# Performance work log

Measured on AMD Instinct MI355X. Metric: run time of the kernel, lower is better.

The kernel has to match this reference:

```python
import jax, jax.numpy as jnp
import numpy as np

B, S, H, F, E, K, R = 1, 1024, 1024, 4096, 8, 2, 16
SCALING = 2.0  # lora_alpha / lora_r = 32 / 16


def setup_inputs() -> dict:
    key = jax.random.key(0)
    ks = jax.random.split(key, 14)
    rnd = lambda i, shape, scale=0.02: (jax.random.normal(ks[i], shape, jnp.float32) * scale)
    return {
        "hidden_states": rnd(0, (B, S, H), 1.0),
        "noise": rnd(1, (B * S, E), 1.0),          # stands in for torch.randn_like(logits)
        "w_route": rnd(2, (H, E)),                   # gate.topkroute_linear.weight^T
        "w_noise": rnd(3, (H, E)),                   # gate.noise_linear.weight^T
        "w_gate": rnd(4, (H, F)),                    # shared mlp gate_proj
        "w_up": rnd(5, (H, F)),                      # shared mlp up_proj
        "w_down": rnd(6, (F, H)),                    # shared mlp down_proj
        "a_gate": rnd(7, (E, H, R)),                 # per-expert LoRA A/B on gate_proj
        "b_gate": rnd(8, (E, R, F)),
        "a_up": rnd(9, (E, H, R)),
        "b_up": rnd(10, (E, R, F)),
        "a_down": rnd(11, (E, F, R)),
        "b_down": rnd(12, (E, R, H)),
    }


def reference(hidden_states, noise, w_route, w_noise, w_gate, w_up, w_down,
              a_gate, b_gate, a_up, b_up, a_down, b_down):
    Bx, Sx, Hx = hidden_states.shape
    x = hidden_states.reshape(-1, Hx)                       # [T, H]
    T = x.shape[0]

    # NoisyTopkRouter
    logits = x @ w_route                                     # [T, E]
    noise_logits = x @ w_noise
    router_logits = logits + noise * jax.nn.softplus(noise_logits)

    # softmax in fp32, top-k, renormalize
    probs = jax.nn.softmax(router_logits.astype(jnp.float32), axis=-1)
    rw, sel = jax.lax.top_k(probs, K)                        # [T, K]
    rw = rw / rw.sum(axis=-1, keepdims=True)
    rw = rw.astype(x.dtype)

    # dense per-(token, expert) combine weights (equiv. to the gather/index_add loop)
    wdense = jnp.zeros((T, E), x.dtype).at[jnp.arange(T)[:, None], sel].add(rw)  # [T, E]

    # LoRA experts (Mixtral MLP shared `mlp` + per-expert low-rank adapters), vectorized over E
    gate = jnp.einsum('th,hf->tf', x, w_gate)[None] + SCALING * jnp.einsum('th,ehr,erf->etf', x, a_gate, b_gate)  # [E,T,F]
    up = jnp.einsum('th,hf->tf', x, w_up)[None] + SCALING * jnp.einsum('th,ehr,erf->etf', x, a_up, b_up)          # [E,T,F]
    act = jax.nn.silu(gate) * up                                                                                   # [E,T,F]
    down = jnp.einsum('etf,fh->eth', act, w_down) + SCALING * jnp.einsum('etf,efr,erh->eth', act, a_down, b_down)  # [E,T,H]

    out = jnp.einsum('te,eth->th', wdense, down)             # scatter-add combine
    return out.reshape(Bx, Sx, Hx), router_logits
```

## Files before the change

### kernel.cpp

```cpp
#include <hip/hip_runtime.h>
#include <hip/hip_bf16.h>

typedef __hip_bfloat16 bf16;
typedef __attribute__((ext_vector_type(4))) float f32x4;
typedef __attribute__((ext_vector_type(8))) __bf16 bf16x8;

#define T_TOK 1024
#define HDIM 1024
#define FDIM 4096
#define NEXP 8
#define RLORA 16
#define LSCALE 2.0f
#define N1 8448
#define N2 1152
#define SPLITK2 4
#define ACT_NCHUNK 8

__device__ inline float b2f(bf16 v) { return __bfloat162float(v); }
__device__ inline bf16 f2b(float v) { return __float2bfloat16(v); }
__device__ inline ushort f2u(float v) { return __builtin_bit_cast(ushort, __float2bfloat16(v)); }
__device__ inline float u2f(ushort v) { return __bfloat162float(__builtin_bit_cast(bf16, v)); }
__device__ inline float lo2f(unsigned w) { return __builtin_bit_cast(float, w << 16); }
__device__ inline float hi2f(unsigned w) { return __builtin_bit_cast(float, w & 0xffff0000u); }

typedef const __attribute__((address_space(1))) unsigned int* gptr_t;
typedef __attribute__((address_space(3))) unsigned int* lptr_t;
__device__ __forceinline__ void glds16(const void* g, void* l) {
    __builtin_amdgcn_global_load_lds((gptr_t)g, (lptr_t)l, 16, 0, 0);
}

__global__ __launch_bounds__(256) void router_kernel(
    const float* __restrict__ x, const float* __restrict__ noise,
    const float* __restrict__ w_route, const float* __restrict__ w_noise,
    float* __restrict__ rl_out, int* __restrict__ SEL, float* __restrict__ WTS,
    int* __restrict__ CNT, int* __restrict__ LIST)
{
    const int t = blockIdx.x, tid = threadIdx.x;
    const float* xr = x + t * HDIM;
    float acc[16];
#pragma unroll
    for (int j = 0; j < 16; j++) acc[j] = 0.f;
    for (int h = tid; h < HDIM; h += 256) {
        float xv = xr[h];
        const float* wr = w_route + h * NEXP;
        const float* wn = w_noise + h * NEXP;
#pragma unroll
        for (int j = 0; j < 8; j++) acc[j] += xv * wr[j];
#pragma unroll
        for (int j = 0; j < 8; j++) acc[8 + j] += xv * wn[j];
    }
#pragma unroll
    for (int j = 0; j < 16; j++) {
        for (int off = 32; off > 0; off >>= 1) acc[j] += __shfl_down(acc[j], off, 64);
    }
    __shared__ float red[4][16];
    const int wave = tid >> 6, lane = tid & 63;
    if (lane == 0) {
#pragma unroll
        for (int j = 0; j < 16; j++) red[wave][j] = acc[j];
    }
    __syncthreads();
    if (tid == 0) {
        float rl[8];
#pragma unroll
        for (int j = 0; j < 8; j++) {
            float lg = red[0][j] + red[1][j] + red[2][j] + red[3][j];
            float nl = red[0][8 + j] + red[1][8 + j] + red[2][8 + j] + red[3][8 + j];
            float sp = fmaxf(nl, 0.f) + log1pf(expf(-fabsf(nl)));
            rl[j] = lg + noise[t * NEXP + j] * sp;
            rl_out[t * NEXP + j] = rl[j];
        }
        float m = rl[0];
#pragma unroll
        for (int j = 1; j < 8; j++) m = fmaxf(m, rl[j]);
        float p[8];
#pragma unroll
        for (int j = 0; j < 8; j++) p[j] = expf(rl[j] - m);
        int i1 = 0;
#pragma unroll
        for (int j = 1; j < 8; j++) if (p[j] > p[i1]) i1 = j;
        int i2 = (i1 == 0) ? 1 : 0;
#pragma unroll
        for (int j = 0; j < 8; j++) { if (j != i1 && p[j] > p[i2]) i2 = j; }
        float w1 = p[i1] / (p[i1] + p[i2]);
        float w2 = p[i2] / (p[i1] + p[i2]);
        SEL[t * 2 + 0] = i1; SEL[t * 2 + 1] = i2;
        WTS[t * 2 + 0] = w1; WTS[t * 2 + 1] = w2;
        int idx0 = atomicAdd(&CNT[i1], 1); LIST[i1 * 2048 + idx0] = 2 * t;
        int idx1 = atomicAdd(&CNT[i2], 1); LIST[i2 * 2048 + idx1] = 2 * t + 1;
    }
}

__device__ __forceinline__ void transpose_tile(
    const float* __restrict__ in, ushort* __restrict__ out,
    int rows, int cols, int bx, int by, int tid)
{
    __shared__ float tile[32][33];
    const int tx = tid & 31, ty = tid >> 5;
#pragma unroll
    for (int i = 0; i < 32; i += 8)
        tile[ty + i][tx] = in[(size_t)(by + ty + i) * cols + bx + tx];
    __syncthreads();
#pragma unroll
    for (int i = 0; i < 32; i += 8)
        out[(size_t)(bx + ty + i) * rows + by + tx] = f2u(tile[tx][ty + i]);
}

__global__ __launch_bounds__(256) void prep_kernel(
    const float* __restrict__ x,
    const float* __restrict__ w_gate, const float* __restrict__ w_up,
    const float* __restrict__ w_down,
    const float* __restrict__ a_gate, const float* __restrict__ a_up,
    const float* __restrict__ a_down,
    ushort* __restrict__ XB, ushort* __restrict__ WGUA, ushort* __restrict__ WDA)
{
    const int bid = blockIdx.x, tid = threadIdx.x;
    if (bid < 4096) {
        transpose_tile(w_gate, WGUA, HDIM, FDIM, (bid & 127) * 32, (bid >> 7) * 32, tid);
    } else if (bid < 8192) {
        const int s = bid - 4096;
        transpose_tile(w_up, WGUA + (size_t)4096 * HDIM, HDIM, FDIM, (s & 127) * 32, (s >> 7) * 32, tid);
    } else if (bid < 12288) {
        const int s = bid - 8192;
        transpose_tile(w_down, WDA, FDIM, HDIM, (s & 31) * 32, (s >> 5) * 32, tid);
    } else if (bid < 12544) {
        const int row = bid - 12288;
        const int e = row >> 5, mat = (row >> 4) & 1, r = row & 15;
        const float* src = (mat ? a_up : a_gate) + (size_t)e * HDIM * RLORA;
        ushort* dst = WGUA + (size_t)(8192 + row) * HDIM;
        for (int h = tid; h < HDIM; h += 256) dst[h] = f2u(src[h * RLORA + r]);
    } else if (bid < 12672) {
        const int row = bid - 12544;
        const int e = row >> 4, r = row & 15;
        const float* src = a_down + (size_t)e * FDIM * RLORA;
        ushort* dst = WDA + (size_t)(1024 + row) * FDIM;
        for (int f = tid; f < FDIM; f += 256) dst[f] = f2u(src[f * RLORA + r]);
    } else {
        const int i = (bid - 12672) * 256 + tid;
        const float4 v = *reinterpret_cast<const float4*>(x + (size_t)i * 4);
        ushort4 o;
        o.x = f2u(v.x); o.y = f2u(v.y); o.z = f2u(v.z); o.w = f2u(v.w);
        *reinterpret_cast<ushort4*>(XB + (size_t)i * 4) = o;
    }
}

template <bool OUT_BF16, int SPLITK>
__global__ __launch_bounds__(256) void gemm128(
    const ushort* __restrict__ A, const ushort* __restrict__ Bt,
    void* __restrict__ Cv, int M, int N, int Kd, int ny)
{
    __shared__ __align__(16) ushort sA[128 * 64];
    __shared__ __align__(16) ushort sB[128 * 64];
    const int nwg = gridDim.x;
    const int q = nwg >> 3;
    const int wg = (blockIdx.x & 7) * q + (blockIdx.x >> 3);
    const int bn0 = (wg / ny) * 128, bm0 = (wg % ny) * 128;

    const int tid = threadIdx.x;
    const int wave = tid >> 6, lane = tid & 63;
    const int wm = wave >> 1, wn = wave & 1;

    f32x4 acc[4][4];
#pragma unroll
    for (int m = 0; m < 4; m++)
#pragma unroll
        for (int n = 0; n < 4; n++) acc[m][n] = (f32x4){0.f, 0.f, 0.f, 0.f};

    const int srow = tid >> 3;
    const int sgrp8 = ((tid & 7) ^ (srow & 7)) * 8;

    const int kchunk = Kd / SPLITK;
    const int kbeg = blockIdx.z * kchunk, kend = kbeg + kchunk;
    for (int k0 = kbeg; k0 < kend; k0 += 64) {
#pragma unroll
        for (int i = 0; i < 4; i++) {
            const int row = i * 32 + srow;
            glds16(A + (size_t)(bm0 + row) * Kd + k0 + sgrp8, &sA[i * 2048 + wave * 512]);
            glds16(Bt + (size_t)(bn0 + row) * Kd + k0 + sgrp8, &sB[i * 2048 + wave * 512]);
        }
        __syncthreads();
#pragma unroll
        for (int kk = 0; kk < 2; kk++) {
            bf16x8 af[4], bfr[4];
            const int colb = (kk * 32 + (lane >> 4) * 8) * 2;
#pragma unroll
            for (int m = 0; m < 4; m++) {
                const int row = wm * 64 + m * 16 + (lane & 15);
                af[m] = *reinterpret_cast<const bf16x8*>(
                    (const char*)sA + row * 128 + (colb ^ ((row & 7) << 4)));
            }
#pragma unroll
            for (int n = 0; n < 4; n++) {
                const int row = wn * 64 + n * 16 + (lane & 15);
                bfr[n] = *reinterpret_cast<const bf16x8*>(
                    (const char*)sB + row * 128 + (colb ^ ((row & 7) << 4)));
            }
#pragma unroll
            for (int m = 0; m < 4; m++)
#pragma unroll
                for (int n = 0; n < 4; n++)
                    acc[m][n] = __builtin_amdgcn_mfma_f32_16x16x32_bf16(af[m], bfr[n], acc[m][n], 0, 0, 0);
        }
        __syncthreads();
    }

    const size_t zoff = (size_t)blockIdx.z * M * N;
    const int rg = lane & 15, qg = lane >> 4;
#pragma unroll
    for (int m = 0; m < 4; m++) {
#pragma unroll
        for (int n = 0; n < 4; n++) {
            const int row0 = bm0 + wm * 64 + m * 16 + qg * 4;
            const int col = bn0 + wn * 64 + n * 16 + rg;
#pragma unroll
            for (int j = 0; j < 4; j++) {
                if (OUT_BF16)
                    ((ushort*)Cv)[zoff + (size_t)(row0 + j) * N + col] = f2u(acc[m][n][j]);
                else
                    ((float*)Cv)[zoff + (size_t)(row0 + j) * N + col] = acc[m][n][j];
            }
        }
    }
}

__global__ __launch_bounds__(256) void act3_kernel(
    const ushort* __restrict__ GU,
    const float* __restrict__ b_gate, const float* __restrict__ b_up,
    const int* __restrict__ CNT, const int* __restrict__ LIST,
    unsigned* __restrict__ ACT)
{
    const int e = blockIdx.x, chunk = blockIdx.z;
    const int tid = threadIdx.x;
    const int f = blockIdx.y * 512 + tid * 2;

    float2 bg[16], bu[16];
    {
        const float* bgp = b_gate + (size_t)e * RLORA * FDIM + f;
        const float* bup = b_up + (size_t)e * RLORA * FDIM + f;
#pragma unroll
        for (int r = 0; r < 16; r++) {
            bg[r] = *reinterpret_cast<const float2*>(bgp + (size_t)r * FDIM);
            bu[r] = *reinterpret_cast<const float2*>(bup + (size_t)r * FDIM);
        }
    }

    const int n = __builtin_amdgcn_readfirstlane(CNT[e]);
    for (int i = chunk; i < n; i += ACT_NCHUNK) {
        const int p = __builtin_amdgcn_readfirstlane(LIST[e * 2048 + i]);
        const int t = p >> 1;
        const ushort* gurow = GU + (size_t)t * N1;
        const unsigned* xap = (const unsigned*)(gurow + 8192 + e * 32);
        float xg[16], xu[16];
#pragma unroll
        for (int r = 0; r < 8; r++) {
            unsigned w = xap[r];
            xg[2 * r] = lo2f(w); xg[2 * r + 1] = hi2f(w);
        }
#pragma unroll
        for (int r = 0; r < 8; r++) {
            unsigned w = xap[8 + r];
            xu[2 * r] = lo2f(w); xu[2 * r + 1] = hi2f(w);
        }
        const unsigned gw = *(const unsigned*)(gurow + f);
        const unsigned uw = *(const unsigned*)(gurow + 4096 + f);
        float lg0 = 0.f, lg1 = 0.f, lu0 = 0.f, lu1 = 0.f;
#pragma unroll
        for (int r = 0; r < 16; r++) {
            lg0 += xg[r] * bg[r].x;
            lg1 += xg[r] * bg[r].y;
            lu0 += xu[r] * bu[r].x;
            lu1 += xu[r] * bu[r].y;
        }
        const float gate0 = lo2f(gw) + LSCALE * lg0;
        const float gate1 = hi2f(gw) + LSCALE * lg1;
        const float up0 = lo2f(uw) + LSCALE * lu0;
        const float up1 = hi2f(uw) + LSCALE * lu1;
        const float a0 = (gate0 / (1.f + expf(-gate0))) * up0;
        const float a1 = (gate1 / (1.f + expf(-gate1))) * up1;
        ACT[((size_t)p * FDIM + f) >> 1] = (unsigned)f2u(a0) | ((unsigned)f2u(a1) << 16);
    }
}

__global__ __launch_bounds__(256) void combine2_kernel(
    const float* __restrict__ C2,
    const float* __restrict__ b_down, const int* __restrict__ SEL,
    const float* __restrict__ WTS, float* __restrict__ out)
{
    const int t = blockIdx.x, tid = threadIdx.x;
    const int e0 = SEL[t * 2 + 0], e1 = SEL[t * 2 + 1];
    const float w0 = WTS[t * 2 + 0], w1 = WTS[t * 2 + 1];
    __shared__ float ad0[16], ad1[16];
    if (tid < 16) {
        float v = 0.f;
#pragma unroll
        for (int z = 0; z < SPLITK2; z++)
            v += C2[((size_t)z * 2048 + 2 * t) * N2 + 1024 + e0 * 16 + tid];
        ad0[tid] = v;
    } else if (tid < 32) {
        float v = 0.f;
#pragma unroll
        for (int z = 0; z < SPLITK2; z++)
            v += C2[((size_t)z * 2048 + 2 * t + 1) * N2 + 1024 + e1 * 16 + (tid - 16)];
        ad1[tid - 16] = v;
    }
    __syncthreads();
    const float* B0 = b_down + (size_t)e0 * RLORA * HDIM;
    const float* B1 = b_down + (size_t)e1 * RLORA * HDIM;
    for (int h = tid; h < HDIM; h += 256) {
        float v0 = 0.f, v1 = 0.f;
#pragma unroll
        for (int z = 0; z < SPLITK2; z++) {
            v0 += C2[((size_t)z * 2048 + 2 * t) * N2 + h];
            v1 += C2[((size_t)z * 2048 + 2 * t + 1) * N2 + h];
        }
        float l0 = 0.f, l1 = 0.f;
#pragma unroll
        for (int r = 0; r < 16; r++) {
            l0 += ad0[r] * B0[r * HDIM + h];
            l1 += ad1[r] * B1[r * HDIM + h];
        }
        out[(size_t)t * HDIM + h] = w0 * (v0 + LSCALE * l0) + w1 * (v1 + LSCALE * l1);
    }
}

extern "C" void kernel_launch(void* const* d_in, const int* in_sizes, int n_in,
                              void* d_out, int out_size, void* d_ws, size_t ws_size,
                              hipStream_t stream) {
    (void)in_sizes; (void)n_in; (void)out_size; (void)ws_size;
    const float* x       = (const float*)d_in[0];
    const float* noise   = (const float*)d_in[1];
    const float* w_route = (const float*)d_in[2];
    const float* w_noise = (const float*)d_in[3];
    const float* w_gate  = (const float*)d_in[4];
    const float* w_up    = (const float*)d_in[5];
    const float* w_down  = (const float*)d_in[6];
    const float* a_gate  = (const float*)d_in[7];
    const float* b_gate  = (const float*)d_in[8];
    const float* a_up    = (const float*)d_in[9];
    const float* b_up    = (const float*)d_in[10];
    const float* a_down  = (const float*)d_in[11];
    const float* b_down  = (const float*)d_in[12];
    float* out    = (float*)d_out;
    float* rl_out = out + (size_t)T_TOK * HDIM;

    char* ws = (char*)d_ws;
    float*  C2   = (float*)(ws);
    ushort* WGUA = (ushort*)(ws + (size_t)(18 << 20));
    bf16*   ACT  = (bf16*)(ws + (size_t)(36 << 20));
    ushort* WDA  = (ushort*)(ws + (size_t)(52 << 20));
    ushort* XB   = (ushort*)(ws + (size_t)(62 << 20));
    ushort* C1b  = (ushort*)(ws + (size_t)(64 << 20));
    int*    LIST = (int*)(ws + (size_t)(81 << 20));
    int*    CNT  = (int*)(ws + (size_t)(81 << 20) + (1 << 17));
    int*    SEL  = (int*)(ws + (size_t)(81 << 20) + (1 << 17) + 4096);
    float*  WTS  = (float*)(ws + (size_t)(81 << 20) + (1 << 17) + 16384);

    hipMemsetAsync(CNT, 0, NEXP * sizeof(int), stream);

    router_kernel<<<T_TOK, 256, 0, stream>>>(x, noise, w_route, w_noise, rl_out, SEL, WTS, CNT, LIST);

    prep_kernel<<<13696, 256, 0, stream>>>(x, w_gate, w_up, w_down, a_gate, a_up, a_down,
                                           XB, WGUA, WDA);

    gemm128<true, 1><<<dim3((N1 / 128) * (T_TOK / 128), 1, 1), 256, 0, stream>>>(
        XB, WGUA, C1b, T_TOK, N1, HDIM, T_TOK / 128);

    act3_kernel<<<dim3(NEXP, FDIM / 512, ACT_NCHUNK), 256, 0, stream>>>(
        C1b, b_gate, b_up, CNT, LIST, (unsigned*)ACT);

    gemm128<false, SPLITK2><<<dim3((N2 / 128) * (2 * T_TOK / 128), 1, SPLITK2), 256, 0, stream>>>(
        (const ushort*)ACT, WDA, C2, 2 * T_TOK, N2, FDIM, 2 * T_TOK / 128);

    combine2_kernel<<<T_TOK, 256, 0, stream>>>(C2, b_down, SEL, WTS, out);
}
```

Before: 170.1 us.

## Double-buffer GEMM shared-memory tiles and store split-K partials in bf16

The GEMM kernel now uses two LDS buffers for the A and B tiles and issues the next K-tile's global-to-LDS loads before computing on the current tile, so memory latency overlaps with MFMA work. The second GEMM's split-K partial sums are also written as bf16 instead of fp32, which halves that intermediate's write and read traffic in the combine kernel. In exchange, LDS use per block doubles to 64KB, which may reduce occupancy. Rounding the partials to bf16 before they are summed loses some precision.

```diff
diff --git a/kernel.cpp b/kernel.cpp
--- a/kernel.cpp
+++ b/kernel.cpp
@@ -144,13 +144,13 @@
     }
 }
 
-template <bool OUT_BF16, int SPLITK>
+template <bool OUT_BF16, bool PART_BF16, int SPLITK>
 __global__ __launch_bounds__(256) void gemm128(
     const ushort* __restrict__ A, const ushort* __restrict__ Bt,
     void* __restrict__ Cv, int M, int N, int Kd, int ny)
 {
-    __shared__ __align__(16) ushort sA[128 * 64];
-    __shared__ __align__(16) ushort sB[128 * 64];
+    __shared__ __align__(16) ushort sA[2][128 * 64];
+    __shared__ __align__(16) ushort sB[2][128 * 64];
     const int nwg = gridDim.x;
     const int q = nwg >> 3;
     const int wg = (blockIdx.x & 7) * q + (blockIdx.x >> 3);
@@ -170,15 +170,26 @@
     const int sgrp8 = ((tid & 7) ^ (srow & 7)) * 8;
 
     const int kchunk = Kd / SPLITK;
-    const int kbeg = blockIdx.z * kchunk, kend = kbeg + kchunk;
-    for (int k0 = kbeg; k0 < kend; k0 += 64) {
-#pragma unroll
-        for (int i = 0; i < 4; i++) {
-            const int row = i * 32 + srow;
-            glds16(A + (size_t)(bm0 + row) * Kd + k0 + sgrp8, &sA[i * 2048 + wave * 512]);
-            glds16(Bt + (size_t)(bn0 + row) * Kd + k0 + sgrp8, &sB[i * 2048 + wave * 512]);
-        }
+    const int kbeg = blockIdx.z * kchunk;
+    const int nt = kchunk >> 6;
+
+#define STAGE(buf, kk)                                                              \
+    {                                                                               \
+        _Pragma("unroll")                                                           \
+        for (int i = 0; i < 4; i++) {                                               \
+            const int row = i * 32 + srow;                                          \
+            glds16(A + (size_t)(bm0 + row) * Kd + (kk) + sgrp8,                     \
+                   &sA[buf][i * 2048 + wave * 512]);                                \
+            glds16(Bt + (size_t)(bn0 + row) * Kd + (kk) + sgrp8,                    \
+                   &sB[buf][i * 2048 + wave * 512]);                                \
+        }                                                                           \
+    }
+
+    STAGE(0, kbeg)
+    for (int t = 0; t < nt; ++t) {
+        const int cur = t & 1;
         __syncthreads();
+        if (t + 1 < nt) STAGE(cur ^ 1, kbeg + (t + 1) * 64)
 #pragma unroll
         for (int kk = 0; kk < 2; kk++) {
             bf16x8 af[4], bfr[4];
@@ -187,13 +198,13 @@
             for (int m = 0; m < 4; m++) {
                 const int row = wm * 64 + m * 16 + (lane & 15);
                 af[m] = *reinterpret_cast<const bf16x8*>(
-                    (const char*)sA + row * 128 + (colb ^ ((row & 7) << 4)));
+                    (const char*)sA[cur] + row * 128 + (colb ^ ((row & 7) << 4)));
             }
 #pragma unroll
             for (int n = 0; n < 4; n++) {
                 const int row = wn * 64 + n * 16 + (lane & 15);
                 bfr[n] = *reinterpret_cast<const bf16x8*>(
-                    (const char*)sB + row * 128 + (colb ^ ((row & 7) << 4)));
+                    (const char*)sB[cur] + row * 128 + (colb ^ ((row & 7) << 4)));
             }
 #pragma unroll
             for (int m = 0; m < 4; m++)
@@ -203,6 +214,7 @@
         }
         __syncthreads();
     }
+#undef STAGE
 
     const size_t zoff = (size_t)blockIdx.z * M * N;
     const int rg = lane & 15, qg = lane >> 4;
@@ -214,7 +226,7 @@
             const int col = bn0 + wn * 64 + n * 16 + rg;
 #pragma unroll
             for (int j = 0; j < 4; j++) {
-                if (OUT_BF16)
+                if (OUT_BF16 || PART_BF16)
                     ((ushort*)Cv)[zoff + (size_t)(row0 + j) * N + col] = f2u(acc[m][n][j]);
                 else
                     ((float*)Cv)[zoff + (size_t)(row0 + j) * N + col] = acc[m][n][j];
@@ -282,7 +294,7 @@
 }
 
 __global__ __launch_bounds__(256) void combine2_kernel(
-    const float* __restrict__ C2,
+    const ushort* __restrict__ C2,
     const float* __restrict__ b_down, const int* __restrict__ SEL,
     const float* __restrict__ WTS, float* __restrict__ out)
 {
@@ -294,13 +306,13 @@
         float v = 0.f;
 #pragma unroll
         for (int z = 0; z < SPLITK2; z++)
-            v += C2[((size_t)z * 2048 + 2 * t) * N2 + 1024 + e0 * 16 + tid];
+            v += u2f(C2[((size_t)z * 2048 + 2 * t) * N2 + 1024 + e0 * 16 + tid]);
         ad0[tid] = v;
     } else if (tid < 32) {
         float v = 0.f;
 #pragma unroll
         for (int z = 0; z < SPLITK2; z++)
-            v += C2[((size_t)z * 2048 + 2 * t + 1) * N2 + 1024 + e1 * 16 + (tid - 16)];
+            v += u2f(C2[((size_t)z * 2048 + 2 * t + 1) * N2 + 1024 + e1 * 16 + (tid - 16)]);
         ad1[tid - 16] = v;
     }
     __syncthreads();
@@ -310,8 +322,8 @@
         float v0 = 0.f, v1 = 0.f;
 #pragma unroll
         for (int z = 0; z < SPLITK2; z++) {
-            v0 += C2[((size_t)z * 2048 + 2 * t) * N2 + h];
-            v1 += C2[((size_t)z * 2048 + 2 * t + 1) * N2 + h];
+            v0 += u2f(C2[((size_t)z * 2048 + 2 * t) * N2 + h]);
+            v1 += u2f(C2[((size_t)z * 2048 + 2 * t + 1) * N2 + h]);
         }
         float l0 = 0.f, l1 = 0.f;
 #pragma unroll
@@ -344,7 +356,7 @@
     float* rl_out = out + (size_t)T_TOK * HDIM;
 
     char* ws = (char*)d_ws;
-    float*  C2   = (float*)(ws);
+    ushort* C2   = (ushort*)(ws);
     ushort* WGUA = (ushort*)(ws + (size_t)(18 << 20));
     bf16*   ACT  = (bf16*)(ws + (size_t)(36 << 20));
     ushort* WDA  = (ushort*)(ws + (size_t)(52 << 20));
@@ -362,13 +374,13 @@
     prep_kernel<<<13696, 256, 0, stream>>>(x, w_gate, w_up, w_down, a_gate, a_up, a_down,
                                            XB, WGUA, WDA);
 
-    gemm128<true, 1><<<dim3((N1 / 128) * (T_TOK / 128), 1, 1), 256, 0, stream>>>(
+    gemm128<true, false, 1><<<dim3((N1 / 128) * (T_TOK / 128), 1, 1), 256, 0, stream>>>(
         XB, WGUA, C1b, T_TOK, N1, HDIM, T_TOK / 128);
 
     act3_kernel<<<dim3(NEXP, FDIM / 512, ACT_NCHUNK), 256, 0, stream>>>(
         C1b, b_gate, b_up, CNT, LIST, (unsigned*)ACT);
 
-    gemm128<false, SPLITK2><<<dim3((N2 / 128) * (2 * T_TOK / 128), 1, SPLITK2), 256, 0, stream>>>(
+    gemm128<false, true, SPLITK2><<<dim3((N2 / 128) * (2 * T_TOK / 128), 1, SPLITK2), 256, 0, stream>>>(
         (const ushort*)ACT, WDA, C2, 2 * T_TOK, N2, FDIM, 2 * T_TOK / 128);
 
     combine2_kernel<<<T_TOK, 256, 0, stream>>>(C2, b_down, SEL, WTS, out);
```

New measurement: 172.9 us. No clear change (+1.7%).
